# Optimization experiments

Hardware: AMD Instinct MI355X
Metric: run time of the kernel (lower is better)

Reference implementation:

```python
import jax, jax.numpy as jnp
import numpy as np

MIN_NORM = 1e-15
BALL_EPS = 4e-3          # float32 boundary eps (HGCN convention), c = 1
RES_LAMBDA = 0.5         # args.res_lambda (global in original repo)
N_HOPS = 2


def _artanh(x):
    x = jnp.clip(x, -1.0 + 1e-7, 1.0 - 1e-7)
    return 0.5 * jnp.log((1.0 + x) / (1.0 - x))


def _norm(x):
    return jnp.clip(jnp.linalg.norm(x, axis=-1, keepdims=True), MIN_NORM, None)


def expmap0(u):
    n = _norm(u)
    return jnp.tanh(n) * u / n


def mobius_add(x, y):
    x2 = jnp.sum(x * x, axis=-1, keepdims=True)
    y2 = jnp.sum(y * y, axis=-1, keepdims=True)
    xy = jnp.sum(x * y, axis=-1, keepdims=True)
    num = (1.0 + 2.0 * xy + y2) * x + (1.0 - x2) * y
    den = jnp.clip(1.0 + 2.0 * xy + x2 * y2, MIN_NORM, None)
    return num / den


def expmap(u, p):
    lam = 2.0 / jnp.clip(1.0 - jnp.sum(p * p, axis=-1, keepdims=True), MIN_NORM, None)
    n = _norm(u)
    second = jnp.tanh(0.5 * lam * n) * u / n
    return mobius_add(p, second)


def logmap(y, p):
    sub = mobius_add(-p, y)
    n = _norm(sub)
    lam = 2.0 / jnp.clip(1.0 - jnp.sum(p * p, axis=-1, keepdims=True), MIN_NORM, None)
    return (2.0 / lam) * _artanh(n) * sub / n


def project(x):
    n = _norm(x)
    maxnorm = 1.0 - BALL_EPS
    return jnp.where(n > maxnorm, x / n * maxnorm, x)


def _l2_normalize(x, eps=1e-12):
    return x / jnp.clip(jnp.linalg.norm(x, axis=-1, keepdims=True), eps, None)


def setup_inputs() -> dict:
    key = jax.random.key(0)
    k1, k2, k3, k4, k5 = jax.random.split(key, 5)
    n_entities, n_relations, latdim, n_edges = 200000, 32, 64, 1000000
    entity_emb = 0.1 * jax.random.normal(k1, (n_entities, latdim), dtype=jnp.float32)
    relation_emb = 0.1 * jax.random.normal(k2, (n_relations, latdim), dtype=jnp.float32)
    head = jax.random.randint(k3, (n_edges,), 0, n_entities)
    tail = jax.random.randint(k4, (n_edges,), 0, n_entities)
    edge_index = jnp.stack([head, tail], axis=0).astype(jnp.int64)
    edge_type = jax.random.randint(k5, (n_edges,), 1, n_relations + 1).astype(jnp.int64)
    return {"entity_emb": entity_emb, "relation_emb": relation_emb,
            "edge_index": edge_index, "edge_type": edge_type}


def _agg(entity_emb, relation_emb, head, tail, relation_type):
    n_entities = entity_emb.shape[0]
    head_emb = entity_emb[head]            # [E, d]
    tail_emb = entity_emb[tail]            # [E, d]
    rel_emb = relation_emb[relation_type]  # [E, d]
    ricci = _l2_normalize(tail_emb + rel_emb)
    hyper_head = expmap0(head_emb)
    hyper_tail = expmap(tail_emb, hyper_head)
    hyper_rel = expmap(rel_emb, hyper_head)
    res = project(mobius_add(hyper_tail, hyper_rel))
    res = logmap(res, hyper_head) + ricci * 1e-7
    res = jax.nn.relu(res)
    # scatter_mean by head index
    sums = jnp.zeros((n_entities, res.shape[-1]), res.dtype).at[head].add(res)
    counts = jnp.zeros((n_entities,), res.dtype).at[head].add(1.0)
    return sums / jnp.clip(counts, 1.0, None)[:, None]


def reference(entity_emb, relation_emb, edge_index, edge_type):
    head, tail = edge_index[0], edge_index[1]
    relation_type = edge_type - 1
    entity_res_emb = entity_emb
    e = entity_emb
    for _ in range(N_HOPS):
        e = _agg(e, relation_emb, head, tail, relation_type)
        e = _l2_normalize(e)  # F.normalize (dropout disabled for determinism)
        entity_res_emb = RES_LAMBDA * entity_res_emb + e
    return entity_res_emb
```

## Files before the change

### kernel.cpp

```cpp
#include <hip/hip_runtime.h>
#include <hip/hip_fp16.h>
#include <cmath>

#define MIN_NORM 1e-15f
#define RCPF(x)  __builtin_amdgcn_rcpf(x)
#define SQRTF(x) __builtin_amdgcn_sqrtf(x)
#define RSQF(x)  __builtin_amdgcn_rsqf(x)

template<int CTRL>
__device__ __forceinline__ float dpp_add(float v) {
    return __int_as_float(__builtin_amdgcn_update_dpp(0, __float_as_int(v), CTRL, 0xF, 0xF, false));
}

__device__ __forceinline__ float rsum16(float v) {
    v += dpp_add<0x121>(v);
    v += dpp_add<0x122>(v);
    v += dpp_add<0x124>(v);
    v += dpp_add<0x128>(v);
    return v;
}

__device__ __forceinline__ float rsum8(float v) {
    v += dpp_add<0xB1>(v);
    v += dpp_add<0x4E>(v);
    v += dpp_add<0x141>(v);
    return v;
}

__device__ __forceinline__ float tanh_fast(float x) {
    float ex = __expf(fminf(2.f * x, 30.f));
    return (ex - 1.f) * RCPF(ex + 1.f);
}

__global__ __launch_bounds__(256) void k_pass1(
    const int*    __restrict__ head,
    const float4* __restrict__ ent,
    const float4* __restrict__ rel,
    int*     __restrict__ C,
    float2*  __restrict__ Th1,
    float2*  __restrict__ Tt1,
    float2*  __restrict__ RelC1,
    float2*  __restrict__ RelC2,
    __half2* __restrict__ EH2,
    __half2* __restrict__ RelH2,
    float ILAM2, int E, int N, int NR, int EB, int PG)
{
    int b = (int)blockIdx.x;
    if (b < EB) {
        int i = b * 256 + (int)threadIdx.x;
        if (i < E) atomicAdd(&C[head[i]], 1);
    } else if (b < EB + PG) {
        int gid = ((b - EB) * 256 + (int)threadIdx.x) >> 4;
        int g   = (int)threadIdx.x & 15;
        if (gid >= N) return;
        float4 v = ent[(size_t)gid * 16 + g];
        EH2[(size_t)gid * 32 + 2 * g]     = __floats2half2_rn(v.x, v.y);
        EH2[(size_t)gid * 32 + 2 * g + 1] = __floats2half2_rn(v.z, v.w);
        float n2 = rsum16(v.x * v.x + v.y * v.y + v.z * v.z + v.w * v.w);
        if (g == 0) {
            float nh     = fmaxf(SQRTF(fmaxf(n2, 0.f)), MIN_NORM);
            float inv_nh = RCPF(nh);
            float th     = tanh_fast(nh);
            Th1[gid] = make_float2(th * inv_nh, th * th);
            Tt1[gid] = make_float2(nh, inv_nh);
        }
    } else {
        int gid = ((b - EB - PG) * 256 + (int)threadIdx.x) >> 4;
        int g   = (int)threadIdx.x & 15;
        if (gid >= NR) return;
        float4 v = rel[(size_t)gid * 16 + g];
        RelH2[(size_t)gid * 32 + 2 * g]     = __floats2half2_rn(v.x, v.y);
        RelH2[(size_t)gid * 32 + 2 * g + 1] = __floats2half2_rn(v.z, v.w);
        float n2 = rsum16(v.x * v.x + v.y * v.y + v.z * v.z + v.w * v.w);
        if (g == 0) {
            float nr = fmaxf(SQRTF(n2), MIN_NORM);
            float inv_nr = RCPF(nr);
            RelC1[gid] = make_float2(nr, inv_nr);
            float thr2 = tanh_fast(ILAM2 * nr);
            RelC2[gid] = make_float2(thr2 * inv_nr, thr2 * thr2);
        }
    }
}

__global__ __launch_bounds__(256) void k_scan1(const int* __restrict__ C,
                                               int* __restrict__ T,
                                               int* __restrict__ BS,
                                               int* __restrict__ DH, int N) {
    __shared__ int lds[256];
    __shared__ int lh[64];
    if (threadIdx.x < 64) lh[threadIdx.x] = 0;
    int i = blockIdx.x * 256 + (int)threadIdx.x;
    int v = (i < N) ? C[i] : 0;
    lds[threadIdx.x] = v;
    __syncthreads();
    for (int off = 1; off < 256; off <<= 1) {
        int add = (threadIdx.x >= (unsigned)off) ? lds[threadIdx.x - off] : 0;
        __syncthreads();
        lds[threadIdx.x] += add;
        __syncthreads();
    }
    if (i < N) {
        T[i] = lds[threadIdx.x];
        int bd = 63 - min(v, 63);
        atomicAdd(&lh[bd], 1);
    }
    if (threadIdx.x == 255) BS[blockIdx.x] = lds[255];
    __syncthreads();
    if (threadIdx.x < 64 && lh[threadIdx.x] > 0)
        atomicAdd(&DH[threadIdx.x], lh[threadIdx.x]);
}

__global__ __launch_bounds__(1024) void k_scan2(int* __restrict__ BS,
                                                const int* __restrict__ DH,
                                                int* __restrict__ DB, int nb) {
    if (blockIdx.x == 0) {
        __shared__ int lds[1024];
        int v = ((int)threadIdx.x < nb) ? BS[threadIdx.x] : 0;
        lds[threadIdx.x] = v;
        __syncthreads();
        for (int off = 1; off < 1024; off <<= 1) {
            int add = (threadIdx.x >= (unsigned)off) ? lds[threadIdx.x - off] : 0;
            __syncthreads();
            lds[threadIdx.x] += add;
            __syncthreads();
        }
        if ((int)threadIdx.x < nb) BS[threadIdx.x] = lds[threadIdx.x] - v;
    } else {
        __shared__ int lds[64];
        if (threadIdx.x >= 64) return;
        int t = (int)threadIdx.x;
        int v = DH[t];
        lds[t] = v;
        __syncthreads();
        for (int off = 1; off < 64; off <<= 1) {
            int add = (t >= off) ? lds[t - off] : 0;
            __syncthreads();
            lds[t] += add;
            __syncthreads();
        }
        DB[t] = lds[t] - v;
    }
}

__global__ __launch_bounds__(256) void k_scan3(const int* __restrict__ C,
                                               const int* __restrict__ T,
                                               const int* __restrict__ BS,
                                               int2* __restrict__ OC,
                                               int* __restrict__ P, int N) {
    int i = blockIdx.x * 256 + (int)threadIdx.x;
    if (i < N) {
        int c = C[i];
        int beg = T[i] - c + BS[blockIdx.x];
        OC[i] = make_int2(beg, c);
        P[i] = beg;
    }
}

__global__ __launch_bounds__(256) void k_pass2(
    const int* __restrict__ C,
    int*       __restrict__ DB,
    int*       __restrict__ perm,
    const int* __restrict__ head,
    const int* __restrict__ tail,
    const int* __restrict__ etype,
    int*       __restrict__ P,
    int*       __restrict__ rec,
    int N, int E, int NB, int SLICES)
{
    int b = (int)blockIdx.x;
    if (b < NB) {
        __shared__ int lh[64];
        __shared__ int lbase[64];
        if (threadIdx.x < 64) lh[threadIdx.x] = 0;
        __syncthreads();
        int i = b * 256 + (int)threadIdx.x;
        int bd = -1, lr = 0;
        if (i < N) {
            bd = 63 - min(C[i], 63);
            lr = atomicAdd(&lh[bd], 1);
        }
        __syncthreads();
        if (threadIdx.x < 64 && lh[threadIdx.x] > 0)
            lbase[threadIdx.x] = atomicAdd(&DB[threadIdx.x], lh[threadIdx.x]);
        __syncthreads();
        if (bd >= 0) perm[lbase[bd] + lr] = i;
    } else {
        int region = b & 7;
        int slice  = (b - NB) >> 3;
        int rlo = (int)(((long long)region * N) >> 3);
        int rhi = (int)(((long long)(region + 1) * N) >> 3);
        int step = 256 * SLICES;
        for (int i = slice * 256 + (int)threadIdx.x; i < E; i += step) {
            int h = head[i];
            int t = tail[i];
            int et = etype[i];
            if (h >= rlo && h < rhi) {
                int pos = atomicAdd(&P[h], 1);
                rec[pos] = t | ((et - 1) << 20);
            }
        }
    }
}

template<bool HOP2>
__global__ __launch_bounds__(256) void rgat_hop_kernel(
    const __half2* __restrict__ e2,
    const __half2* __restrict__ rel2,
    const float2*  __restrict__ Th1,
    const float2*  __restrict__ Tt1,
    const float2*  __restrict__ Tt2,
    const float2*  __restrict__ RelC1,
    const float2*  __restrict__ RelC2,
    const int*     __restrict__ rec,
    const int2*    __restrict__ OC,
    const int*     __restrict__ perm,
    const float2*  __restrict__ entf2,
    float2*        __restrict__ outf2,
    __half2*       __restrict__ Ah2w,
    float2*        __restrict__ Tt2w,
    float SCP2, float P2C, float ILAM2, int N)
{
    int tid  = blockIdx.x * 256 + (int)threadIdx.x;
    int slot = tid >> 3;
    int l    = (int)threadIdx.x & 7;
    bool act = slot < N;
    int h    = perm[act ? slot : 0];

    int2 oc = OC[h];
    int beg = act ? oc.x : 0;
    int end = act ? (oc.x + oc.y) : 0;

    const __half2* hrow = e2 + (size_t)h * 32 + l;
    float hv[8];
#pragma unroll
    for (int k = 0; k < 4; ++k) {
        float2 f = __half22float2(hrow[8 * k]);
        hv[2 * k] = f.x; hv[2 * k + 1] = f.y;
    }

    float scp, p2;
    if constexpr (HOP2) {
        scp = SCP2; p2 = P2C;
    } else {
        float2 th = Th1[h];
        scp = th.x; p2 = th.y;
    }
    float bet  = fmaxf(1.f - p2, MIN_NORM);
    float ilam = RCPF(bet);
    float bet2 = bet * bet;

    float acc[8];
#pragma unroll
    for (int k = 0; k < 8; ++k) acc[k] = 0.f;

    float tA[8], rA[8], tB[8], rB[8];
    float2 tvA, rvA, tvB, rvB;

    auto LD = [&](int i, float* T, float* R, float2& TV, float2& RV) {
        int rc = rec[i];
        int ti = rc & 0xFFFFF;
        int ri = rc >> 20;
        const __half2* tr = e2   + (size_t)ti * 32 + l;
        const __half2* rr = rel2 + (size_t)ri * 32 + l;
#pragma unroll
        for (int k = 0; k < 4; ++k) {
            float2 ft = __half22float2(tr[8 * k]);
            float2 fr = __half22float2(rr[8 * k]);
            T[2 * k] = ft.x; T[2 * k + 1] = ft.y;
            R[2 * k] = fr.x; R[2 * k + 1] = fr.y;
        }
        if constexpr (HOP2) { TV = Tt2[ti]; RV = RelC2[ri]; }
        else               { TV = Tt1[ti]; RV = RelC1[ri]; }
    };

    auto COMPUTE = [&](const float* t, const float* r, float2 tv, float2 rv) {
        float pht = 0.f, phr = 0.f, ptr_ = 0.f;
#pragma unroll
        for (int k = 0; k < 8; ++k) {
            pht  += hv[k] * t[k];
            phr  += hv[k] * r[k];
            ptr_ += t[k] * r[k];
        }
        float ht  = rsum8(pht);
        float hr  = rsum8(phr);
        float ttr = rsum8(ptr_);

        float sct, y2t, scr, y2r;
        if constexpr (HOP2) {
            sct = tv.x; y2t = tv.y;
            scr = rv.x; y2r = rv.y;
        } else {
            float tht = tanh_fast(ilam * tv.x);
            sct = tht * tv.y;  y2t = tht * tht;
            float thr_ = tanh_fast(ilam * rv.x);
            scr = thr_ * rv.y; y2r = thr_ * thr_;
        }

        float xyt = scp * sct * ht;
        float xyr = scp * scr * hr;

        float alt  = fmaf(2.f, xyt, 1.f + y2t);
        float dent = fmaxf(fmaf(p2, y2t, fmaf(2.f, xyt, 1.f)), MIN_NORM);
        float alr  = fmaf(2.f, xyr, 1.f + y2r);
        float denr = fmaxf(fmaf(p2, y2r, fmaf(2.f, xyr, 1.f)), MIN_NORM);
        float iS   = RCPF(dent * denr);
        float idt  = iS * denr;
        float idr  = iS * dent;

        float a2 = (alt * alt * p2 + 2.f * alt * bet * xyt + bet * bet * y2t) * idt * idt;
        float pa = fmaf(bet, xyt, alt * p2) * idt;
        float b2 = (alr * alr * p2 + 2.f * alr * bet * xyr + bet * bet * y2r) * idr * idr;
        float pb = fmaf(bet, xyr, alr * p2) * idr;

        float ytyr = sct * scr * ttr;
        float ab = (alt * alr * p2 + alt * bet * xyr + bet * alr * xyt + bet * bet * ytyr) * idt * idr;

        float am   = fmaf(2.f, ab, 1.f + b2);
        float bm   = 1.f - a2;
        float denm = fmaxf(fmaf(a2, b2, fmaf(2.f, ab, 1.f)), MIN_NORM);
        float idm  = RCPF(denm);
        float m2  = (am * am * a2 + 2.f * am * bm * ab + bm * bm * b2) * idm * idm;
        float pmv = fmaf(am, pa, bm * pb) * idm;

        const float maxn  = 1.f - 4e-3f;
        const float maxn2 = maxn * maxn;
        float irm = RSQF(fmaxf(m2, 1e-30f));
        float sc  = (m2 > maxn2) ? (maxn * irm) : 1.f;
        m2  *= sc * sc;
        pmv *= sc;

        float cs   = fmaf(-2.f, pmv, 1.f + m2);
        float dens = fmaxf(fmaf(p2, m2, fmaf(-2.f, pmv, 1.f)), MIN_NORM);
        float ids  = RCPF(dens);
        float s2  = fmaxf((cs * cs * p2 - 2.f * cs * bet * pmv + bet * bet * m2) * ids * ids, 1e-30f);
        float irs = RSQF(s2);
        float ns  = s2 * irs;
        float xa  = fminf(ns, 1.f - 1e-7f);
        float ath = 0.5f * __logf((1.f + xa) * RCPF(1.f - xa));
        float lgs = bet * ath * irs;

        float X  = am * idt;
        float Y  = bm * idr;
        float G  = idm * sc;
        float W  = lgs * ids;
        float WG = W * G;
        float Kt = WG * X * bet2 * sct;
        float Kr = WG * Y * bet2 * scr;
        float Z  = WG * bet * fmaf(X, alt, Y * alr);
        float Kh = scp * (Z - W * cs);

#pragma unroll
        for (int k = 0; k < 8; ++k)
            acc[k] += fmaxf(fmaf(Kh, hv[k], fmaf(Kt, t[k], Kr * r[k])), 0.f);
    };

    int i = beg;
    if (i < end) {
        LD(i, tA, rA, tvA, rvA);
        while (true) {
            if (i + 1 < end) LD(i + 1, tB, rB, tvB, rvB);
            COMPUTE(tA, rA, tvA, rvA);
            ++i;
            if (i >= end) break;
            if (i + 1 < end) LD(i + 1, tA, rA, tvA, rvA);
            COMPUTE(tB, rB, tvB, rvB);
            ++i;
            if (i >= end) break;
        }
    }

    if (!act) return;

    float pn = 0.f;
#pragma unroll
    for (int k = 0; k < 8; ++k) pn += acc[k] * acc[k];
    float n2 = rsum8(pn);
    float sn = SQRTF(n2);
    float inv = RCPF(fmaxf(sn, 1e-12f));

    if constexpr (HOP2) {
        const float2* en = entf2 + (size_t)h * 32 + l;
        float2*       dd = outf2 + (size_t)h * 32 + l;
#pragma unroll
        for (int k = 0; k < 4; ++k) {
            float2 e = en[8 * k];
            float2 o;
            o.x = fmaf(0.25f, e.x, fmaf(0.5f, hv[2 * k],     acc[2 * k]     * inv));
            o.y = fmaf(0.25f, e.y, fmaf(0.5f, hv[2 * k + 1], acc[2 * k + 1] * inv));
            dd[8 * k] = o;
        }
    } else {
        __half2* ad = Ah2w + (size_t)h * 32 + l;
#pragma unroll
        for (int k = 0; k < 4; ++k)
            ad[8 * k] = __floats2half2_rn(acc[2 * k] * inv, acc[2 * k + 1] * inv);
        if (l == 0) {
            float nv = sn * inv;
            float nt = fmaxf(nv, MIN_NORM);
            float tht2 = tanh_fast(ILAM2 * nt);
            Tt2w[h] = make_float2(tht2 * RCPF(nt), tht2 * tht2);
        }
    }
}

extern "C" void kernel_launch(void* const* d_in, const int* in_sizes, int n_in,
                              void* d_out, int out_size, void* d_ws, size_t ws_size,
                              hipStream_t stream)
{
    const float* ent   = (const float*)d_in[0];
    const float* rel   = (const float*)d_in[1];
    const int*   eidx  = (const int*)d_in[2];
    const int*   etype = (const int*)d_in[3];

    int E = in_sizes[3];
    int N = in_sizes[0] / 64;
    int NR = in_sizes[1] / 64;
    const int* head = eidx;
    const int* tail = eidx + E;

    double th1d = tanh(1.0);
    float SCP2  = (float)th1d;
    float P2C   = (float)(th1d * th1d);
    float ILAM2 = (float)(1.0 / (1.0 - th1d * th1d));

    __half2* EH2   = (__half2*)d_ws;
    __half2* Ah2   = EH2 + (size_t)N * 32;
    __half2* RelH2 = Ah2 + (size_t)N * 32;
    int*     rec   = (int*)(RelH2 + (size_t)NR * 32);
    int2*    OC    = (int2*)(rec + E);
    int*     P     = (int*)(OC + N);
    int*     C     = P + N;
    int*     DH    = C + N;
    int*     T     = DH + 64;
    int*     BS    = T + N;
    int*     DB    = BS + 1024;
    int*     perm  = DB + 64;
    float2*  Th1   = (float2*)(perm + N);
    float2*  Tt1   = Th1 + N;
    float2*  Tt2   = Tt1 + N;
    float2*  RelC1 = Tt2 + N;
    float2*  RelC2 = RelC1 + NR;

    int NB = (N + 255) / 256;
    int EB = (E + 255) / 256;
    int PG = (N * 16 + 255) / 256;
    int RG = (NR * 16 + 255) / 256;
    const int SLICES = 104;

    float* out = (float*)d_out;
    dim3 blk(256);
    int hopGrid = (N * 8 + 255) / 256;

    (void)hipMemsetAsync(C, 0, (size_t)(N + 64) * sizeof(int), stream);

    k_pass1<<<EB + PG + RG, blk, 0, stream>>>(
        head, (const float4*)ent, (const float4*)rel,
        C, Th1, Tt1, RelC1, RelC2, EH2, RelH2, ILAM2, E, N, NR, EB, PG);

    k_scan1<<<NB, blk, 0, stream>>>(C, T, BS, DH, N);
    k_scan2<<<2, 1024, 0, stream>>>(BS, DH, DB, NB);
    k_scan3<<<NB, blk, 0, stream>>>(C, T, BS, OC, P, N);

    k_pass2<<<NB + 8 * SLICES, blk, 0, stream>>>(
        C, DB, perm, head, tail, etype, P, rec, N, E, NB, SLICES);

    rgat_hop_kernel<false><<<hopGrid, blk, 0, stream>>>(
        EH2, RelH2, Th1, Tt1, Tt2, RelC1, RelC2, rec, OC, perm,
        nullptr, nullptr, Ah2, Tt2, SCP2, P2C, ILAM2, N);

    rgat_hop_kernel<true><<<hopGrid, blk, 0, stream>>>(
        Ah2, RelH2, Th1, Tt1, Tt2, RelC1, RelC2, rec, OC, perm,
        (const float2*)ent, (float2*)out, nullptr, nullptr, SCP2, P2C, ILAM2, N);
}
```

Before: 258.4 us.

## Vectorize row gathers to 16-byte loads and deepen edge prefetch to four

Each lane now owns 8 contiguous features and loads them with one 16-byte load in place of four strided 4-byte loads. This applies to head, tail and relation rows and to the output/entity stores. The edge loop is deepened from double to quad buffering, using masked loads past the end so two edges are in flight ahead of compute. This cuts load instruction count and increases memory-level parallelism, at the cost of more registers and wasted masked work on short rows.

```diff
diff --git a/kernel.cpp b/kernel.cpp
--- a/kernel.cpp
+++ b/kernel.cpp
@@ -214,8 +214,8 @@
     const int*     __restrict__ rec,
     const int2*    __restrict__ OC,
     const int*     __restrict__ perm,
-    const float2*  __restrict__ entf2,
-    float2*        __restrict__ outf2,
+    const float*   __restrict__ entf,
+    float*         __restrict__ outf,
     __half2*       __restrict__ Ah2w,
     float2*        __restrict__ Tt2w,
     float SCP2, float P2C, float ILAM2, int N)
@@ -230,12 +230,15 @@
     int beg = act ? oc.x : 0;
     int end = act ? (oc.x + oc.y) : 0;
 
-    const __half2* hrow = e2 + (size_t)h * 32 + l;
+    float4 hraw = *reinterpret_cast<const float4*>(e2 + (size_t)h * 32 + 4 * l);
     float hv[8];
-#pragma unroll
-    for (int k = 0; k < 4; ++k) {
-        float2 f = __half22float2(hrow[8 * k]);
-        hv[2 * k] = f.x; hv[2 * k + 1] = f.y;
+    {
+        const __half2* hp = reinterpret_cast<const __half2*>(&hraw);
+#pragma unroll
+        for (int k = 0; k < 4; ++k) {
+            float2 f = __half22float2(hp[k]);
+            hv[2 * k] = f.x; hv[2 * k + 1] = f.y;
+        }
     }
 
     float scp, p2;
@@ -253,27 +256,35 @@
 #pragma unroll
     for (int k = 0; k < 8; ++k) acc[k] = 0.f;
 
-    float tA[8], rA[8], tB[8], rB[8];
-    float2 tvA, rvA, tvB, rvB;
-
-    auto LD = [&](int i, float* T, float* R, float2& TV, float2& RV) {
-        int rc = rec[i];
+    float4 tA, rA, tB, rB, tC, rC, tD, rD;
+    float2 tvA, rvA, tvB, rvB, tvC, rvC, tvD, rvD;
+    float mA, mB, mC, mD;
+
+    auto LD = [&](int i, float4& T, float4& R, float2& TV, float2& RV, float& M) {
+        bool ok = i < end;
+        int ii = ok ? i : 0;
+        int rc = rec[ii];
         int ti = rc & 0xFFFFF;
         int ri = rc >> 20;
-        const __half2* tr = e2   + (size_t)ti * 32 + l;
-        const __half2* rr = rel2 + (size_t)ri * 32 + l;
-#pragma unroll
-        for (int k = 0; k < 4; ++k) {
-            float2 ft = __half22float2(tr[8 * k]);
-            float2 fr = __half22float2(rr[8 * k]);
-            T[2 * k] = ft.x; T[2 * k + 1] = ft.y;
-            R[2 * k] = fr.x; R[2 * k + 1] = fr.y;
-        }
+        T = *reinterpret_cast<const float4*>(e2   + (size_t)ti * 32 + 4 * l);
+        R = *reinterpret_cast<const float4*>(rel2 + (size_t)ri * 32 + 4 * l);
         if constexpr (HOP2) { TV = Tt2[ti]; RV = RelC2[ri]; }
         else               { TV = Tt1[ti]; RV = RelC1[ri]; }
+        M = ok ? 1.f : 0.f;
     };
 
-    auto COMPUTE = [&](const float* t, const float* r, float2 tv, float2 rv) {
+    auto COMPUTE = [&](const float4& T4, const float4& R4, float2 tv, float2 rv, float msk) {
+        float t[8], r[8];
+        const __half2* tp = reinterpret_cast<const __half2*>(&T4);
+        const __half2* rp = reinterpret_cast<const __half2*>(&R4);
+#pragma unroll
+        for (int k = 0; k < 4; ++k) {
+            float2 ft = __half22float2(tp[k]);
+            float2 fr = __half22float2(rp[k]);
+            t[2 * k] = ft.x; t[2 * k + 1] = ft.y;
+            r[2 * k] = fr.x; r[2 * k + 1] = fr.y;
+        }
+
         float pht = 0.f, phr = 0.f, ptr_ = 0.f;
 #pragma unroll
         for (int k = 0; k < 8; ++k) {
@@ -351,20 +362,25 @@
 
 #pragma unroll
         for (int k = 0; k < 8; ++k)
-            acc[k] += fmaxf(fmaf(Kh, hv[k], fmaf(Kt, t[k], Kr * r[k])), 0.f);
+            acc[k] += fmaxf(fmaf(Kh, hv[k], fmaf(Kt, t[k], Kr * r[k])), 0.f) * msk;
     };
 
     int i = beg;
     if (i < end) {
-        LD(i, tA, rA, tvA, rvA);
+        LD(i,     tA, rA, tvA, rvA, mA);
+        LD(i + 1, tB, rB, tvB, rvB, mB);
         while (true) {
-            if (i + 1 < end) LD(i + 1, tB, rB, tvB, rvB);
-            COMPUTE(tA, rA, tvA, rvA);
-            ++i;
+            LD(i + 2, tC, rC, tvC, rvC, mC);
+            LD(i + 3, tD, rD, tvD, rvD, mD);
+            COMPUTE(tA, rA, tvA, rvA, mA);
+            COMPUTE(tB, rB, tvB, rvB, mB);
+            i += 2;
             if (i >= end) break;
-            if (i + 1 < end) LD(i + 1, tA, rA, tvA, rvA);
-            COMPUTE(tB, rB, tvB, rvB);
-            ++i;
+            LD(i + 2, tA, rA, tvA, rvA, mA);
+            LD(i + 3, tB, rB, tvB, rvB, mB);
+            COMPUTE(tC, rC, tvC, rvC, mC);
+            COMPUTE(tD, rD, tvD, rvD, mD);
+            i += 2;
             if (i >= end) break;
         }
     }
@@ -379,21 +395,27 @@
     float inv = RCPF(fmaxf(sn, 1e-12f));
 
     if constexpr (HOP2) {
-        const float2* en = entf2 + (size_t)h * 32 + l;
-        float2*       dd = outf2 + (size_t)h * 32 + l;
-#pragma unroll
-        for (int k = 0; k < 4; ++k) {
-            float2 e = en[8 * k];
-            float2 o;
-            o.x = fmaf(0.25f, e.x, fmaf(0.5f, hv[2 * k],     acc[2 * k]     * inv));
-            o.y = fmaf(0.25f, e.y, fmaf(0.5f, hv[2 * k + 1], acc[2 * k + 1] * inv));
-            dd[8 * k] = o;
-        }
+        const float4* en = reinterpret_cast<const float4*>(entf + (size_t)h * 64 + 8 * l);
+        float4 e0 = en[0], e1 = en[1];
+        float4 o0, o1;
+        o0.x = fmaf(0.25f, e0.x, fmaf(0.5f, hv[0], acc[0] * inv));
+        o0.y = fmaf(0.25f, e0.y, fmaf(0.5f, hv[1], acc[1] * inv));
+        o0.z = fmaf(0.25f, e0.z, fmaf(0.5f, hv[2], acc[2] * inv));
+        o0.w = fmaf(0.25f, e0.w, fmaf(0.5f, hv[3], acc[3] * inv));
+        o1.x = fmaf(0.25f, e1.x, fmaf(0.5f, hv[4], acc[4] * inv));
+        o1.y = fmaf(0.25f, e1.y, fmaf(0.5f, hv[5], acc[5] * inv));
+        o1.z = fmaf(0.25f, e1.z, fmaf(0.5f, hv[6], acc[6] * inv));
+        o1.w = fmaf(0.25f, e1.w, fmaf(0.5f, hv[7], acc[7] * inv));
+        float4* dd = reinterpret_cast<float4*>(outf + (size_t)h * 64 + 8 * l);
+        dd[0] = o0;
+        dd[1] = o1;
     } else {
-        __half2* ad = Ah2w + (size_t)h * 32 + l;
+        float4 st;
+        __half2* sp = reinterpret_cast<__half2*>(&st);
 #pragma unroll
         for (int k = 0; k < 4; ++k)
-            ad[8 * k] = __floats2half2_rn(acc[2 * k] * inv, acc[2 * k + 1] * inv);
+            sp[k] = __floats2half2_rn(acc[2 * k] * inv, acc[2 * k + 1] * inv);
+        *reinterpret_cast<float4*>(Ah2w + (size_t)h * 32 + 4 * l) = st;
         if (l == 0) {
             float nv = sn * inv;
             float nt = fmaxf(nv, MIN_NORM);
@@ -470,5 +492,5 @@
 
     rgat_hop_kernel<true><<<hopGrid, blk, 0, stream>>>(
         Ah2, RelH2, Th1, Tt1, Tt2, RelC1, RelC2, rec, OC, perm,
-        (const float2*)ent, (float2*)out, nullptr, nullptr, SCP2, P2C, ILAM2, N);
-}
+        ent, out, nullptr, nullptr, SCP2, P2C, ILAM2, N);
+}
```

Result: slower. 277.1 us (+7.2%).
